# Kernel tuning notes

Hardware: AMD Instinct MI355X
Metric: run time of the kernel (lower is better)

Reference implementation:

```python
import jax, jax.numpy as jnp
import numpy as np

NUM_NODES = 512
HEADS = 4
IN_F = 256
OUT_F = 128
EPS = 1e-5


def _layernorm(x, g, b):
    mu = jnp.mean(x, axis=-1, keepdims=True)
    var = jnp.mean(jnp.square(x - mu), axis=-1, keepdims=True)
    return (x - mu) * jax.lax.rsqrt(var + EPS) * g + b


def setup_inputs() -> dict:
    key = jax.random.key(0)
    ks = jax.random.split(key, 16)
    N = 32 * NUM_NODES
    E = 262144
    s = 0.05
    return {
        "x": jax.random.normal(ks[0], (N, IN_F), jnp.float32),
        "edge_index": jax.random.randint(ks[1], (2, E), 0, N, jnp.int64),
        "W_l": jax.random.normal(ks[2], (IN_F, HEADS * OUT_F), jnp.float32) * s,
        "W_r": jax.random.normal(ks[3], (IN_F, HEADS * OUT_F), jnp.float32) * s,
        "att": jax.random.normal(ks[4], (HEADS, OUT_F), jnp.float32) * s,
        "gat_bias": jnp.zeros((OUT_F,), jnp.float32),
        "gat_gamma": jnp.ones((OUT_F,), jnp.float32),
        "gat_beta": jnp.zeros((OUT_F,), jnp.float32),
        "cnn_W": jax.random.normal(ks[5], (IN_F, OUT_F), jnp.float32) * s,
        "cnn_b": jnp.zeros((OUT_F,), jnp.float32),
        "conv_W": jax.random.normal(ks[6], (OUT_F, OUT_F, 7), jnp.float32) * s,
        "conv_b": jnp.zeros((OUT_F,), jnp.float32),
        "cnn_gamma": jnp.ones((OUT_F,), jnp.float32),
        "cnn_beta": jnp.zeros((OUT_F,), jnp.float32),
        "res_W": jax.random.normal(ks[7], (IN_F, OUT_F), jnp.float32) * s,
        "res_b": jnp.zeros((OUT_F,), jnp.float32),
        "fuse_gamma": jnp.ones((OUT_F,), jnp.float32),
        "fuse_beta": jnp.zeros((OUT_F,), jnp.float32),
    }


def reference(x, edge_index, W_l, W_r, att, gat_bias, gat_gamma, gat_beta,
              cnn_W, cnn_b, conv_W, conv_b, cnn_gamma, cnn_beta,
              res_W, res_b, fuse_gamma, fuse_beta):
    N = x.shape[0]
    B = N // NUM_NODES
    # --- GATv2 branch (add self-loops like PyG default) ---
    loop = jnp.arange(N, dtype=edge_index.dtype)
    src = jnp.concatenate([edge_index[0], loop])
    dst = jnp.concatenate([edge_index[1], loop])
    x_l = (x @ W_l).reshape(N, HEADS, OUT_F)
    x_r = (x @ W_r).reshape(N, HEADS, OUT_F)
    e = x_l[src] + x_r[dst]                      # [E+N, H, F]
    e = jnp.where(e > 0, e, 0.2 * e)             # leaky_relu, slope 0.2
    score = jnp.einsum('ehf,hf->eh', e, att)     # [E+N, H]
    m = jax.ops.segment_max(score, dst, num_segments=N)
    ex = jnp.exp(score - m[dst])
    denom = jax.ops.segment_sum(ex, dst, num_segments=N)
    alpha = ex / denom[dst]
    agg = jax.ops.segment_sum(alpha[:, :, None] * x_l[src], dst, num_segments=N)
    h_gat = jnp.mean(agg, axis=1) + gat_bias     # concat=False -> head mean
    h_gat = jnp.where(h_gat > 0, h_gat, 0.01 * h_gat)  # nn.LeakyReLU default
    h_gat = _layernorm(h_gat, gat_gamma, gat_beta)
    # --- CNN branch ---
    xc = x @ cnn_W + cnn_b                       # [N, F]
    xc = xc.reshape(B, NUM_NODES, OUT_F).transpose(0, 2, 1)  # [B, F, L]
    hc = jax.lax.conv_general_dilated(xc, conv_W, window_strides=(1,),
                                      padding=[(3, 3)],
                                      dimension_numbers=('NCW', 'OIW', 'NCW'))
    hc = hc + conv_b[None, :, None]
    hc = hc.transpose(0, 2, 1).reshape(N, OUT_F)
    hc = jax.nn.relu(hc)
    hc = _layernorm(hc, cnn_gamma, cnn_beta)
    # --- fuse + residual ---
    h = h_gat + hc + (x @ res_W + res_b)
    return _layernorm(h, fuse_gamma, fuse_beta)
```

## Files before the change

### kernel.cpp

```cpp
#include <hip/hip_runtime.h>
#include <hip/hip_bf16.h>
#include <math.h>

#define IN_F 256
#define OUT_F 128
#define HEADS 4
#define HF 512
#define NCAT 1280

typedef __hip_bfloat16 bf16;
typedef unsigned short ushort_t;

using bf16x8 = __attribute__((ext_vector_type(8))) short;
using f32x4  = __attribute__((ext_vector_type(4))) float;

__device__ __forceinline__ float bflo(unsigned u) { return __uint_as_float(u << 16); }
__device__ __forceinline__ float bfhi(unsigned u) { return __uint_as_float(u & 0xffff0000u); }
__device__ __forceinline__ float bf2f(ushort_t u) { return __uint_as_float((unsigned)u << 16); }
__device__ __forceinline__ ushort_t f2bf(float f) {
    __hip_bfloat16 h = __float2bfloat16(f);
    return *reinterpret_cast<ushort_t*>(&h);
}

__device__ __forceinline__ void gload16(const void* g, void* l) {
    __builtin_amdgcn_global_load_lds(
        (const __attribute__((address_space(1))) unsigned int*)g,
        (__attribute__((address_space(3))) unsigned int*)l, 16, 0, 0);
}

template <int CTRL>
__device__ __forceinline__ float dpp_add(float s) {
    int t = __builtin_amdgcn_update_dpp(0, __float_as_int(s), CTRL, 0xf, 0xf, true);
    return s + __int_as_float(t);
}
__device__ __forceinline__ float rowsum16(float s) {
    s = dpp_add<0x121>(s);
    s = dpp_add<0x122>(s);
    s = dpp_add<0x124>(s);
    s = dpp_add<0x128>(s);
    return s;
}

__global__ __launch_bounds__(256) void prep_kernel(
    const float* __restrict__ x, ushort_t* __restrict__ xb, int n_cvt,
    const float* __restrict__ Wl, const float* __restrict__ Wr,
    const float* __restrict__ Wc, const float* __restrict__ Wres,
    const float* __restrict__ Wconv,
    ushort_t* __restrict__ Wt, ushort_t* __restrict__ Wt2,
    const int* __restrict__ ei, int* __restrict__ counts, int E,
    int g1, int g2) {
    int b = blockIdx.x;
    if (b < g1) {
        int i = (b * 256 + threadIdx.x) * 8;
        if (i >= n_cvt) return;
        float4 a = *(const float4*)(x + i);
        float4 c = *(const float4*)(x + i + 4);
        uint4 o;
        o.x = f2bf(a.x) | ((unsigned)f2bf(a.y) << 16);
        o.y = f2bf(a.z) | ((unsigned)f2bf(a.w) << 16);
        o.z = f2bf(c.x) | ((unsigned)f2bf(c.y) << 16);
        o.w = f2bf(c.z) | ((unsigned)f2bf(c.w) << 16);
        *(uint4*)(xb + i) = o;
    } else if (b < g2) {
        int idx = (b - g1) * 256 + threadIdx.x;
        if (idx < NCAT * 256) {
            int n = idx >> 8, k = idx & 255;
            float v;
            if (n < 512)       v = Wl[(size_t)k * 512 + n];
            else if (n < 1024) v = Wr[(size_t)k * 512 + (n - 512)];
            else if (n < 1152) v = Wc[(size_t)k * 128 + (n - 1024)];
            else               v = Wres[(size_t)k * 128 + (n - 1152)];
            Wt[idx] = f2bf(v);
        } else {
            int j = idx - NCAT * 256;
            if (j < 7 * 128 * 128) {
                int k = j >> 14, o = (j >> 7) & 127, i = j & 127;
                Wt2[j] = f2bf(Wconv[((size_t)o * 128 + i) * 7 + k]);
            }
        }
    } else {
        int e = (b - g2) * 256 + threadIdx.x;
        if (e < E) atomicAdd(&counts[ei[E + e]], 1);
    }
}

__global__ __launch_bounds__(256) void mfma_gemm(
    const ushort_t* __restrict__ A,
    const ushort_t* __restrict__ Wt,
    ushort_t* __restrict__ xlb, ushort_t* __restrict__ xrb,
    ushort_t* __restrict__ xcb, ushort_t* __restrict__ resb,
    int M) {
    __shared__ __align__(1024) ushort_t As[128 * 64];
    __shared__ __align__(1024) ushort_t Bs[128 * 64];
    int tid = threadIdx.x;
    int lane = tid & 63, wid = tid >> 6;
    int wr = (wid >> 1) * 64, wc = (wid & 1) * 64;
    int brow = blockIdx.y * 128, bcol = blockIdx.x * 128;
    int srow = lane >> 3;
    int sslot = lane & 7;
    int rl = lane & 15, kq = lane >> 4;
    f32x4 acc[4][4] = {};
    for (int k0 = 0; k0 < 256; k0 += 64) {
        #pragma unroll
        for (int j = 0; j < 4; ++j) {
            int r = (wid * 4 + j) * 8 + srow;
            int sl = sslot ^ (r & 7);
            gload16(A  + (size_t)(brow + r) * 256 + k0 + sl * 8,
                    (char*)As + (wid * 4 + j) * 1024);
            gload16(Wt + (size_t)(bcol + r) * 256 + k0 + sl * 8,
                    (char*)Bs + (wid * 4 + j) * 1024);
        }
        __syncthreads();
        #pragma unroll
        for (int ks = 0; ks < 2; ++ks) {
            int cb = ks * 64 + kq * 16;
            bf16x8 af[4], bfv[4];
            #pragma unroll
            for (int m = 0; m < 4; ++m) {
                int r = wr + m * 16 + rl;
                af[m] = *(const bf16x8*)((const char*)As + r * 128 + (cb ^ ((r & 7) << 4)));
            }
            #pragma unroll
            for (int n = 0; n < 4; ++n) {
                int r = wc + n * 16 + rl;
                bfv[n] = *(const bf16x8*)((const char*)Bs + r * 128 + (cb ^ ((r & 7) << 4)));
            }
            #pragma unroll
            for (int m = 0; m < 4; ++m)
                #pragma unroll
                for (int n = 0; n < 4; ++n)
                    acc[m][n] = __builtin_amdgcn_mfma_f32_16x16x32_bf16(
                        af[m], bfv[n], acc[m][n], 0, 0, 0);
        }
        __syncthreads();
    }
    ushort_t* dstp; int cstride, cb2;
    if (bcol < 512)       { dstp = xlb;  cstride = 512; cb2 = bcol; }
    else if (bcol < 1024) { dstp = xrb;  cstride = 512; cb2 = bcol - 512; }
    else if (bcol < 1152) { dstp = xcb;  cstride = 128; cb2 = bcol - 1024; }
    else                  { dstp = resb; cstride = 128; cb2 = bcol - 1152; }
    int rowb = (lane >> 4) * 4;
    #pragma unroll
    for (int m = 0; m < 4; ++m)
        #pragma unroll
        for (int n = 0; n < 4; ++n) {
            int col = cb2 + wc + n * 16 + rl;
            #pragma unroll
            for (int q = 0; q < 4; ++q) {
                int row = brow + wr + m * 16 + rowb + q;
                dstp[(size_t)row * cstride + col] = f2bf(acc[m][n][q]);
            }
        }
}

__global__ __launch_bounds__(1024) void scan_kernel(
    const int* __restrict__ counts, int* __restrict__ offs,
    int* __restrict__ cursor, int N) {
    __shared__ int wsum[16];
    int t = threadIdx.x;
    int lane = t & 63, w = t >> 6;
    int base = t * 16;
    int local[16], s = 0;
    #pragma unroll
    for (int i = 0; i < 16; ++i) {
        int v = (base + i < N) ? counts[base + i] : 0;
        local[i] = v; s += v;
    }
    int sc = s;
    #pragma unroll
    for (int off = 1; off < 64; off <<= 1) {
        int v = __shfl_up(sc, off);
        if (lane >= off) sc += v;
    }
    if (lane == 63) wsum[w] = sc;
    __syncthreads();
    if (w == 0 && lane < 16) {
        int v = wsum[lane];
        int scv = v;
        #pragma unroll
        for (int off = 1; off < 16; off <<= 1) {
            int u = __shfl_up(scv, off);
            if (lane >= off) scv += u;
        }
        wsum[lane] = scv - v;
    }
    __syncthreads();
    int run = wsum[w] + sc - s;
    #pragma unroll
    for (int i = 0; i < 16; ++i) {
        if (base + i < N) { offs[base + i] = run; cursor[base + i] = run; }
        run += local[i];
    }
}

__global__ __launch_bounds__(256) void scatter_kernel(
    const int* __restrict__ ei, int* __restrict__ cursor,
    int* __restrict__ srcs, int E) {
    int e = blockIdx.x * 256 + threadIdx.x;
    if (e < E) {
        int d = ei[E + e];
        int p = atomicAdd(&cursor[d], 1);
        srcs[p] = ei[e];
    }
}

__global__ __launch_bounds__(256) void gat_fused_kernel(
    const ushort_t* __restrict__ xlb, const ushort_t* __restrict__ xrb,
    const int* __restrict__ srcs, const int* __restrict__ offs,
    const float* __restrict__ att, const float* __restrict__ gat_bias,
    const float* __restrict__ gat_gamma, const float* __restrict__ gat_beta,
    float* __restrict__ hgat_ln, int E, int N) {
    int wid = (blockIdx.x * 256 + threadIdx.x) >> 6;
    int lane = threadIdx.x & 63;
    if (wid >= N) return;
    int d = wid;
    const uint4 rv = ((const uint4*)(xrb + (size_t)d * HF))[lane];
    float xr8[8];
    xr8[0] = bflo(rv.x); xr8[1] = bfhi(rv.x);
    xr8[2] = bflo(rv.y); xr8[3] = bfhi(rv.y);
    xr8[4] = bflo(rv.z); xr8[5] = bfhi(rv.z);
    xr8[6] = bflo(rv.w); xr8[7] = bfhi(rv.w);
    const float LOG2E = 1.44269504f;
    const float4 a0 = ((const float4*)att)[lane * 2];
    const float4 a1 = ((const float4*)att)[lane * 2 + 1];
    const float aw[8] = {a0.x * LOG2E, a0.y * LOG2E, a0.z * LOG2E, a0.w * LOG2E,
                         a1.x * LOG2E, a1.y * LOG2E, a1.z * LOG2E, a1.w * LOG2E};
    float acc[8] = {};
    float dn = 0.f;

    auto process = [&](uint4 lv) {
        float xl8[8];
        xl8[0] = bflo(lv.x); xl8[1] = bfhi(lv.x);
        xl8[2] = bflo(lv.y); xl8[3] = bfhi(lv.y);
        xl8[4] = bflo(lv.z); xl8[5] = bfhi(lv.z);
        xl8[6] = bflo(lv.w); xl8[7] = bfhi(lv.w);
        float s1 = 0.f, s2 = 0.f;
        #pragma unroll
        for (int j = 0; j < 8; ++j) {
            float v = xl8[j] + xr8[j];
            s1 = fmaf(v, aw[j], s1);
            s2 = fmaf(fabsf(v), aw[j], s2);
        }
        float s = fmaf(0.6f, s1, 0.4f * s2);
        s = rowsum16(s);
        float ex = exp2f(s);
        dn += ex;
        #pragma unroll
        for (int j = 0; j < 8; ++j) acc[j] = fmaf(ex, xl8[j], acc[j]);
    };

    process(((const uint4*)(xlb + (size_t)d * HF))[lane]);

    int start = offs[d];
    int end = (d == N - 1) ? E : offs[d + 1];
    int p = start;
    for (; p + 3 < end; p += 4) {
        int s0 = srcs[p], s1 = srcs[p + 1], s2 = srcs[p + 2], s3 = srcs[p + 3];
        uint4 l0 = ((const uint4*)(xlb + (size_t)s0 * HF))[lane];
        uint4 l1 = ((const uint4*)(xlb + (size_t)s1 * HF))[lane];
        uint4 l2 = ((const uint4*)(xlb + (size_t)s2 * HF))[lane];
        uint4 l3 = ((const uint4*)(xlb + (size_t)s3 * HF))[lane];
        process(l0); process(l1); process(l2); process(l3);
    }
    for (; p < end; ++p)
        process(((const uint4*)(xlb + (size_t)srcs[p] * HF))[lane]);

    float inv = 1.f / dn;
    float v[8];
    #pragma unroll
    for (int j = 0; j < 8; ++j) {
        float t2 = acc[j] * inv;
        t2 += __shfl_xor(t2, 16);
        t2 += __shfl_xor(t2, 32);
        v[j] = t2;
    }
    int h = lane >> 4;
    int col = (lane & 15) * 8 + 2 * h;
    float g0 = 0.25f * v[2 * h]     + gat_bias[col];
    float g1 = 0.25f * v[2 * h + 1] + gat_bias[col + 1];
    g0 = g0 > 0.f ? g0 : 0.01f * g0;
    g1 = g1 > 0.f ? g1 : 0.01f * g1;
    float s = g0 + g1;
    #pragma unroll
    for (int off = 32; off; off >>= 1) s += __shfl_xor(s, off);
    float mu = s * (1.f / 128.f);
    float d0 = g0 - mu, d1 = g1 - mu;
    float vs = d0 * d0 + d1 * d1;
    #pragma unroll
    for (int off = 32; off; off >>= 1) vs += __shfl_xor(vs, off);
    float rinv = rsqrtf(vs * (1.f / 128.f) + 1e-5f);
    hgat_ln[(size_t)d * 128 + col]     = d0 * rinv * gat_gamma[col]     + gat_beta[col];
    hgat_ln[(size_t)d * 128 + col + 1] = d1 * rinv * gat_gamma[col + 1] + gat_beta[col + 1];
}

__global__ __launch_bounds__(256) void conv_fuse_kernel(
    const ushort_t* __restrict__ xcb, const float* __restrict__ cnn_b,
    const ushort_t* __restrict__ Wt2,
    const float* __restrict__ hgat_ln, const ushort_t* __restrict__ resb,
    const float* __restrict__ conv_b,
    const float* __restrict__ cnn_gamma, const float* __restrict__ cnn_beta,
    const float* __restrict__ res_b,
    const float* __restrict__ fuse_gamma, const float* __restrict__ fuse_beta,
    float* __restrict__ out) {
    __shared__ ushort_t As[38][136];
    __shared__ __align__(1024) ushort_t Bs[128 * 128];
    __shared__ float hbuf[32][129];
    int tid = threadIdx.x;
    int lane = tid & 63, wid = tid >> 6;
    int wr = (wid >> 1) * 16, wc = (wid & 1) * 64;
    int b = blockIdx.y, l0 = blockIdx.x * 32;
    for (int u = tid; u < 38 * 16; u += 256) {
        int r = u >> 4, seg = u & 15;
        int l = l0 - 3 + r;
        uint4 o4 = make_uint4(0, 0, 0, 0);
        if (l >= 0 && l < 512) {
            uint4 v = *(const uint4*)(xcb + (size_t)(b * 512 + l) * 128 + seg * 8);
            float4 b0 = *(const float4*)(cnn_b + seg * 8);
            float4 b1 = *(const float4*)(cnn_b + seg * 8 + 4);
            o4.x = f2bf(bflo(v.x) + b0.x) | ((unsigned)f2bf(bfhi(v.x) + b0.y) << 16);
            o4.y = f2bf(bflo(v.y) + b0.z) | ((unsigned)f2bf(bfhi(v.y) + b0.w) << 16);
            o4.z = f2bf(bflo(v.z) + b1.x) | ((unsigned)f2bf(bfhi(v.z) + b1.y) << 16);
            o4.w = f2bf(bflo(v.w) + b1.z) | ((unsigned)f2bf(bfhi(v.w) + b1.w) << 16);
        }
        *(uint4*)&As[r][seg * 8] = o4;
    }
    f32x4 acc[4] = {};
    int rl = lane & 15, kb = (lane >> 4) * 8;
    int sr4 = lane >> 4, ss = lane & 15;
    for (int k = 0; k < 7; ++k) {
        __syncthreads();
        #pragma unroll
        for (int j = 0; j < 8; ++j) {
            int r = (wid * 8 + j) * 4 + sr4;
            int sl = ss ^ (r & 15);
            gload16(Wt2 + ((size_t)(k * 128 + r)) * 128 + sl * 8,
                    (char*)Bs + (wid * 8 + j) * 1024);
        }
        __syncthreads();
        #pragma unroll
        for (int kk = 0; kk < 4; ++kk) {
            bf16x8 af = *(const bf16x8*)&As[wr + rl + k][kk * 32 + kb];
            int cbyte = kk * 64 + (lane >> 4) * 16;
            #pragma unroll
            for (int n = 0; n < 4; ++n) {
                int r = wc + n * 16 + rl;
                bf16x8 bfr = *(const bf16x8*)((const char*)Bs + r * 256
                                              + (cbyte ^ ((r & 15) << 4)));
                acc[n] = __builtin_amdgcn_mfma_f32_16x16x32_bf16(af, bfr, acc[n], 0, 0, 0);
            }
        }
    }
    __syncthreads();
    int rowb = (lane >> 4) * 4;
    #pragma unroll
    for (int n = 0; n < 4; ++n) {
        int col = wc + n * 16 + rl;
        float cb = conv_b[col];
        #pragma unroll
        for (int q = 0; q < 4; ++q) {
            int r = wr + rowb + q;
            hbuf[r][col] = fmaxf(acc[n][q] + cb, 0.f);
        }
    }
    __syncthreads();
    for (int r = wid * 8; r < wid * 8 + 8; ++r) {
        int grow = b * 512 + l0 + r;
        float h0 = hbuf[r][lane], h1 = hbuf[r][lane + 64];
        float s = h0 + h1;
        #pragma unroll
        for (int off = 32; off; off >>= 1) s += __shfl_xor(s, off);
        float mu = s * (1.f / 128.f);
        float d0 = h0 - mu, d1 = h1 - mu;
        float vs = d0 * d0 + d1 * d1;
        #pragma unroll
        for (int off = 32; off; off >>= 1) vs += __shfl_xor(vs, off);
        float inv = rsqrtf(vs * (1.f / 128.f) + 1e-5f);
        float hcn0 = d0 * inv * cnn_gamma[lane]      + cnn_beta[lane];
        float hcn1 = d1 * inv * cnn_gamma[lane + 64] + cnn_beta[lane + 64];
        size_t base = (size_t)grow * 128;
        float v0 = hgat_ln[base + lane]      + hcn0
                 + bf2f(resb[base + lane])      + res_b[lane];
        float v1 = hgat_ln[base + lane + 64] + hcn1
                 + bf2f(resb[base + lane + 64]) + res_b[lane + 64];
        s = v0 + v1;
        #pragma unroll
        for (int off = 32; off; off >>= 1) s += __shfl_xor(s, off);
        mu = s * (1.f / 128.f);
        d0 = v0 - mu; d1 = v1 - mu;
        vs = d0 * d0 + d1 * d1;
        #pragma unroll
        for (int off = 32; off; off >>= 1) vs += __shfl_xor(vs, off);
        inv = rsqrtf(vs * (1.f / 128.f) + 1e-5f);
        out[base + lane]      = d0 * inv * fuse_gamma[lane]      + fuse_beta[lane];
        out[base + lane + 64] = d1 * inv * fuse_gamma[lane + 64] + fuse_beta[lane + 64];
    }
}

extern "C" void kernel_launch(void* const* d_in, const int* in_sizes, int n_in,
                              void* d_out, int out_size, void* d_ws, size_t ws_size,
                              hipStream_t stream) {
    const float* x         = (const float*)d_in[0];
    const int*   ei        = (const int*)d_in[1];
    const float* W_l       = (const float*)d_in[2];
    const float* W_r       = (const float*)d_in[3];
    const float* att       = (const float*)d_in[4];
    const float* gat_bias  = (const float*)d_in[5];
    const float* gat_gamma = (const float*)d_in[6];
    const float* gat_beta  = (const float*)d_in[7];
    const float* cnn_W     = (const float*)d_in[8];
    const float* cnn_b     = (const float*)d_in[9];
    const float* conv_W    = (const float*)d_in[10];
    const float* conv_b    = (const float*)d_in[11];
    const float* cnn_gamma = (const float*)d_in[12];
    const float* cnn_beta  = (const float*)d_in[13];
    const float* res_W     = (const float*)d_in[14];
    const float* res_b     = (const float*)d_in[15];
    const float* fuse_gamma= (const float*)d_in[16];
    const float* fuse_beta = (const float*)d_in[17];

    int N = in_sizes[0] / IN_F;
    int E = in_sizes[1] / 2;

    char* ws = (char*)d_ws;
    size_t off = 0;
    ushort_t* xb     = (ushort_t*)(ws + off); off += (size_t)N * IN_F * 2;
    ushort_t* Wt     = (ushort_t*)(ws + off); off += (size_t)NCAT * IN_F * 2;
    ushort_t* Wt2    = (ushort_t*)(ws + off); off += (size_t)7 * 128 * 128 * 2;
    ushort_t* xlb    = (ushort_t*)(ws + off); off += (size_t)N * HF * 2;
    ushort_t* xrb    = (ushort_t*)(ws + off); off += (size_t)N * HF * 2;
    ushort_t* xcb    = (ushort_t*)(ws + off); off += (size_t)N * 128 * 2;
    ushort_t* resb   = (ushort_t*)(ws + off); off += (size_t)N * 128 * 2;
    int*  counts     = (int*)(ws + off);  off += (size_t)N * 4;
    int*  offs       = (int*)(ws + off);  off += (size_t)N * 4;
    int*  cursor     = (int*)(ws + off);  off += (size_t)N * 4;
    int*  srcs       = (int*)(ws + off);  off += (size_t)E * 4;
    float* hgat_ln   = (float*)(ws + off); off += (size_t)N * 128 * 4;

    hipMemsetAsync(counts, 0, (size_t)N * 4, stream);

    dim3 blk(256);
    int n_cvt = N * IN_F;
    int g1 = (n_cvt / 8 + 255) / 256;
    int g2 = g1 + (NCAT * 256 + 7 * 128 * 128 + 255) / 256;
    int g3 = g2 + (E + 255) / 256;
    prep_kernel<<<g3, blk, 0, stream>>>(x, xb, n_cvt,
        W_l, W_r, cnn_W, res_W, conv_W, Wt, Wt2, ei, counts, E, g1, g2);

    scan_kernel<<<1, 1024, 0, stream>>>(counts, offs, cursor, N);
    scatter_kernel<<<(E + 255) / 256, blk, 0, stream>>>(ei, cursor, srcs, E);

    mfma_gemm<<<dim3(NCAT / 128, N / 128), blk, 0, stream>>>(
        xb, Wt, xlb, xrb, xcb, resb, N);

    gat_fused_kernel<<<(N + 3) / 4, blk, 0, stream>>>(
        xlb, xrb, srcs, offs, att, gat_bias, gat_gamma, gat_beta, hgat_ln, E, N);

    conv_fuse_kernel<<<dim3(16, 32), blk, 0, stream>>>(
        xcb, cnn_b, Wt2, hgat_ln, resb, conv_b, cnn_gamma, cnn_beta,
        res_b, fuse_gamma, fuse_beta, (float*)d_out);
}
```

Measured before the change: 144.1 us.

## Reorder conv and GAT stages, fuse final layernorm into GAT kernel

Runs the conv+layernorm kernel first and writes its normalized output as bf16, then moves the residual add and final fuse layernorm into the GAT aggregation kernel. The fp32 hgat_ln intermediate is gone, so its write and re-read are no longer needed. The GAT inner math now uses two-wide float vectors, which may map to packed FMA instructions. The bf16 rounding of the CNN-branch output adds some precision loss.

Measured after the change: 142.9 us. No clear change (-0.8%).

```diff
diff --git a/kernel.cpp b/kernel.cpp
--- a/kernel.cpp
+++ b/kernel.cpp
@@ -13,6 +13,7 @@
 
 using bf16x8 = __attribute__((ext_vector_type(8))) short;
 using f32x4  = __attribute__((ext_vector_type(4))) float;
+using f32v2  = __attribute__((ext_vector_type(2))) float;
 
 __device__ __forceinline__ float bflo(unsigned u) { return __uint_as_float(u << 16); }
 __device__ __forceinline__ float bfhi(unsigned u) { return __uint_as_float(u & 0xffff0000u); }
@@ -204,104 +205,11 @@
     }
 }
 
-__global__ __launch_bounds__(256) void gat_fused_kernel(
-    const ushort_t* __restrict__ xlb, const ushort_t* __restrict__ xrb,
-    const int* __restrict__ srcs, const int* __restrict__ offs,
-    const float* __restrict__ att, const float* __restrict__ gat_bias,
-    const float* __restrict__ gat_gamma, const float* __restrict__ gat_beta,
-    float* __restrict__ hgat_ln, int E, int N) {
-    int wid = (blockIdx.x * 256 + threadIdx.x) >> 6;
-    int lane = threadIdx.x & 63;
-    if (wid >= N) return;
-    int d = wid;
-    const uint4 rv = ((const uint4*)(xrb + (size_t)d * HF))[lane];
-    float xr8[8];
-    xr8[0] = bflo(rv.x); xr8[1] = bfhi(rv.x);
-    xr8[2] = bflo(rv.y); xr8[3] = bfhi(rv.y);
-    xr8[4] = bflo(rv.z); xr8[5] = bfhi(rv.z);
-    xr8[6] = bflo(rv.w); xr8[7] = bfhi(rv.w);
-    const float LOG2E = 1.44269504f;
-    const float4 a0 = ((const float4*)att)[lane * 2];
-    const float4 a1 = ((const float4*)att)[lane * 2 + 1];
-    const float aw[8] = {a0.x * LOG2E, a0.y * LOG2E, a0.z * LOG2E, a0.w * LOG2E,
-                         a1.x * LOG2E, a1.y * LOG2E, a1.z * LOG2E, a1.w * LOG2E};
-    float acc[8] = {};
-    float dn = 0.f;
-
-    auto process = [&](uint4 lv) {
-        float xl8[8];
-        xl8[0] = bflo(lv.x); xl8[1] = bfhi(lv.x);
-        xl8[2] = bflo(lv.y); xl8[3] = bfhi(lv.y);
-        xl8[4] = bflo(lv.z); xl8[5] = bfhi(lv.z);
-        xl8[6] = bflo(lv.w); xl8[7] = bfhi(lv.w);
-        float s1 = 0.f, s2 = 0.f;
-        #pragma unroll
-        for (int j = 0; j < 8; ++j) {
-            float v = xl8[j] + xr8[j];
-            s1 = fmaf(v, aw[j], s1);
-            s2 = fmaf(fabsf(v), aw[j], s2);
-        }
-        float s = fmaf(0.6f, s1, 0.4f * s2);
-        s = rowsum16(s);
-        float ex = exp2f(s);
-        dn += ex;
-        #pragma unroll
-        for (int j = 0; j < 8; ++j) acc[j] = fmaf(ex, xl8[j], acc[j]);
-    };
-
-    process(((const uint4*)(xlb + (size_t)d * HF))[lane]);
-
-    int start = offs[d];
-    int end = (d == N - 1) ? E : offs[d + 1];
-    int p = start;
-    for (; p + 3 < end; p += 4) {
-        int s0 = srcs[p], s1 = srcs[p + 1], s2 = srcs[p + 2], s3 = srcs[p + 3];
-        uint4 l0 = ((const uint4*)(xlb + (size_t)s0 * HF))[lane];
-        uint4 l1 = ((const uint4*)(xlb + (size_t)s1 * HF))[lane];
-        uint4 l2 = ((const uint4*)(xlb + (size_t)s2 * HF))[lane];
-        uint4 l3 = ((const uint4*)(xlb + (size_t)s3 * HF))[lane];
-        process(l0); process(l1); process(l2); process(l3);
-    }
-    for (; p < end; ++p)
-        process(((const uint4*)(xlb + (size_t)srcs[p] * HF))[lane]);
-
-    float inv = 1.f / dn;
-    float v[8];
-    #pragma unroll
-    for (int j = 0; j < 8; ++j) {
-        float t2 = acc[j] * inv;
-        t2 += __shfl_xor(t2, 16);
-        t2 += __shfl_xor(t2, 32);
-        v[j] = t2;
-    }
-    int h = lane >> 4;
-    int col = (lane & 15) * 8 + 2 * h;
-    float g0 = 0.25f * v[2 * h]     + gat_bias[col];
-    float g1 = 0.25f * v[2 * h + 1] + gat_bias[col + 1];
-    g0 = g0 > 0.f ? g0 : 0.01f * g0;
-    g1 = g1 > 0.f ? g1 : 0.01f * g1;
-    float s = g0 + g1;
-    #pragma unroll
-    for (int off = 32; off; off >>= 1) s += __shfl_xor(s, off);
-    float mu = s * (1.f / 128.f);
-    float d0 = g0 - mu, d1 = g1 - mu;
-    float vs = d0 * d0 + d1 * d1;
-    #pragma unroll
-    for (int off = 32; off; off >>= 1) vs += __shfl_xor(vs, off);
-    float rinv = rsqrtf(vs * (1.f / 128.f) + 1e-5f);
-    hgat_ln[(size_t)d * 128 + col]     = d0 * rinv * gat_gamma[col]     + gat_beta[col];
-    hgat_ln[(size_t)d * 128 + col + 1] = d1 * rinv * gat_gamma[col + 1] + gat_beta[col + 1];
-}
-
-__global__ __launch_bounds__(256) void conv_fuse_kernel(
+__global__ __launch_bounds__(256) void conv_ln_kernel(
     const ushort_t* __restrict__ xcb, const float* __restrict__ cnn_b,
-    const ushort_t* __restrict__ Wt2,
-    const float* __restrict__ hgat_ln, const ushort_t* __restrict__ resb,
-    const float* __restrict__ conv_b,
+    const ushort_t* __restrict__ Wt2, const float* __restrict__ conv_b,
     const float* __restrict__ cnn_gamma, const float* __restrict__ cnn_beta,
-    const float* __restrict__ res_b,
-    const float* __restrict__ fuse_gamma, const float* __restrict__ fuse_beta,
-    float* __restrict__ out) {
+    ushort_t* __restrict__ hcn_ln) {
     __shared__ ushort_t As[38][136];
     __shared__ __align__(1024) ushort_t Bs[128 * 128];
     __shared__ float hbuf[32][129];
@@ -375,25 +283,121 @@
         #pragma unroll
         for (int off = 32; off; off >>= 1) vs += __shfl_xor(vs, off);
         float inv = rsqrtf(vs * (1.f / 128.f) + 1e-5f);
-        float hcn0 = d0 * inv * cnn_gamma[lane]      + cnn_beta[lane];
-        float hcn1 = d1 * inv * cnn_gamma[lane + 64] + cnn_beta[lane + 64];
         size_t base = (size_t)grow * 128;
-        float v0 = hgat_ln[base + lane]      + hcn0
-                 + bf2f(resb[base + lane])      + res_b[lane];
-        float v1 = hgat_ln[base + lane + 64] + hcn1
-                 + bf2f(resb[base + lane + 64]) + res_b[lane + 64];
-        s = v0 + v1;
-        #pragma unroll
-        for (int off = 32; off; off >>= 1) s += __shfl_xor(s, off);
-        mu = s * (1.f / 128.f);
-        d0 = v0 - mu; d1 = v1 - mu;
-        vs = d0 * d0 + d1 * d1;
-        #pragma unroll
-        for (int off = 32; off; off >>= 1) vs += __shfl_xor(vs, off);
-        inv = rsqrtf(vs * (1.f / 128.f) + 1e-5f);
-        out[base + lane]      = d0 * inv * fuse_gamma[lane]      + fuse_beta[lane];
-        out[base + lane + 64] = d1 * inv * fuse_gamma[lane + 64] + fuse_beta[lane + 64];
-    }
+        hcn_ln[base + lane]      = f2bf(d0 * inv * cnn_gamma[lane]      + cnn_beta[lane]);
+        hcn_ln[base + lane + 64] = f2bf(d1 * inv * cnn_gamma[lane + 64] + cnn_beta[lane + 64]);
+    }
+}
+
+__global__ __launch_bounds__(256) void gat_final_kernel(
+    const ushort_t* __restrict__ xlb, const ushort_t* __restrict__ xrb,
+    const int* __restrict__ srcs, const int* __restrict__ offs,
+    const float* __restrict__ att, const float* __restrict__ gat_bias,
+    const float* __restrict__ gat_gamma, const float* __restrict__ gat_beta,
+    const ushort_t* __restrict__ hcn_ln, const ushort_t* __restrict__ resb,
+    const float* __restrict__ res_b,
+    const float* __restrict__ fuse_gamma, const float* __restrict__ fuse_beta,
+    float* __restrict__ out, int E, int N) {
+    int wid = (blockIdx.x * 256 + threadIdx.x) >> 6;
+    int lane = threadIdx.x & 63;
+    if (wid >= N) return;
+    int d = wid;
+    const uint4 rv = ((const uint4*)(xrb + (size_t)d * HF))[lane];
+    f32v2 xr2[4];
+    xr2[0] = f32v2{bflo(rv.x), bfhi(rv.x)};
+    xr2[1] = f32v2{bflo(rv.y), bfhi(rv.y)};
+    xr2[2] = f32v2{bflo(rv.z), bfhi(rv.z)};
+    xr2[3] = f32v2{bflo(rv.w), bfhi(rv.w)};
+    const float LOG2E = 1.44269504f;
+    const float4 a0 = ((const float4*)att)[lane * 2];
+    const float4 a1 = ((const float4*)att)[lane * 2 + 1];
+    f32v2 aw2[4] = {f32v2{a0.x, a0.y} * LOG2E, f32v2{a0.z, a0.w} * LOG2E,
+                    f32v2{a1.x, a1.y} * LOG2E, f32v2{a1.z, a1.w} * LOG2E};
+    f32v2 acc2[4] = {};
+    float dn = 0.f;
+
+    auto process = [&](uint4 lv) {
+        f32v2 xl2[4];
+        xl2[0] = f32v2{bflo(lv.x), bfhi(lv.x)};
+        xl2[1] = f32v2{bflo(lv.y), bfhi(lv.y)};
+        xl2[2] = f32v2{bflo(lv.z), bfhi(lv.z)};
+        xl2[3] = f32v2{bflo(lv.w), bfhi(lv.w)};
+        f32v2 s1 = {0.f, 0.f}, s2 = {0.f, 0.f};
+        #pragma unroll
+        for (int j = 0; j < 4; ++j) {
+            f32v2 v = xl2[j] + xr2[j];
+            s1 = __builtin_elementwise_fma(v, aw2[j], s1);
+            s2 = __builtin_elementwise_fma(__builtin_elementwise_abs(v), aw2[j], s2);
+        }
+        float s = fmaf(0.6f, s1.x + s1.y, 0.4f * (s2.x + s2.y));
+        s = rowsum16(s);
+        float ex = exp2f(s);
+        dn += ex;
+        f32v2 exv = {ex, ex};
+        #pragma unroll
+        for (int j = 0; j < 4; ++j)
+            acc2[j] = __builtin_elementwise_fma(exv, xl2[j], acc2[j]);
+    };
+
+    process(((const uint4*)(xlb + (size_t)d * HF))[lane]);
+
+    int start = offs[d];
+    int end = (d == N - 1) ? E : offs[d + 1];
+    int p = start;
+    for (; p + 3 < end; p += 4) {
+        int s0 = srcs[p], s1 = srcs[p + 1], s2 = srcs[p + 2], s3 = srcs[p + 3];
+        uint4 l0 = ((const uint4*)(xlb + (size_t)s0 * HF))[lane];
+        uint4 l1 = ((const uint4*)(xlb + (size_t)s1 * HF))[lane];
+        uint4 l2 = ((const uint4*)(xlb + (size_t)s2 * HF))[lane];
+        uint4 l3 = ((const uint4*)(xlb + (size_t)s3 * HF))[lane];
+        process(l0); process(l1); process(l2); process(l3);
+    }
+    for (; p < end; ++p)
+        process(((const uint4*)(xlb + (size_t)srcs[p] * HF))[lane]);
+
+    float inv = 1.f / dn;
+    float v[8];
+    #pragma unroll
+    for (int j = 0; j < 4; ++j) {
+        float tx = acc2[j].x * inv, ty = acc2[j].y * inv;
+        tx += __shfl_xor(tx, 16); tx += __shfl_xor(tx, 32);
+        ty += __shfl_xor(ty, 16); ty += __shfl_xor(ty, 32);
+        v[2 * j] = tx; v[2 * j + 1] = ty;
+    }
+    int h = lane >> 4;
+    int col = (lane & 15) * 8 + 2 * h;
+    float g0 = 0.25f * v[2 * h]     + gat_bias[col];
+    float g1 = 0.25f * v[2 * h + 1] + gat_bias[col + 1];
+    g0 = g0 > 0.f ? g0 : 0.01f * g0;
+    g1 = g1 > 0.f ? g1 : 0.01f * g1;
+    float s = g0 + g1;
+    #pragma unroll
+    for (int off = 32; off; off >>= 1) s += __shfl_xor(s, off);
+    float mu = s * (1.f / 128.f);
+    float d0 = g0 - mu, d1 = g1 - mu;
+    float vs = d0 * d0 + d1 * d1;
+    #pragma unroll
+    for (int off = 32; off; off >>= 1) vs += __shfl_xor(vs, off);
+    float rinv = rsqrtf(vs * (1.f / 128.f) + 1e-5f);
+    float hg0 = d0 * rinv * gat_gamma[col]     + gat_beta[col];
+    float hg1 = d1 * rinv * gat_gamma[col + 1] + gat_beta[col + 1];
+    size_t base = (size_t)d * 128 + col;
+    unsigned hcu = *(const unsigned*)(hcn_ln + base);
+    unsigned rsu = *(const unsigned*)(resb + base);
+    float v0 = hg0 + bflo(hcu) + bflo(rsu) + res_b[col];
+    float v1 = hg1 + bfhi(hcu) + bfhi(rsu) + res_b[col + 1];
+    s = v0 + v1;
+    #pragma unroll
+    for (int off = 32; off; off >>= 1) s += __shfl_xor(s, off);
+    mu = s * (1.f / 128.f);
+    d0 = v0 - mu; d1 = v1 - mu;
+    vs = d0 * d0 + d1 * d1;
+    #pragma unroll
+    for (int off = 32; off; off >>= 1) vs += __shfl_xor(vs, off);
+    rinv = rsqrtf(vs * (1.f / 128.f) + 1e-5f);
+    float2 o2 = make_float2(d0 * rinv * fuse_gamma[col]     + fuse_beta[col],
+                            d1 * rinv * fuse_gamma[col + 1] + fuse_beta[col + 1]);
+    *(float2*)(out + base) = o2;
 }
 
 extern "C" void kernel_launch(void* const* d_in, const int* in_sizes, int n_in,
@@ -430,11 +434,11 @@
     ushort_t* xrb    = (ushort_t*)(ws + off); off += (size_t)N * HF * 2;
     ushort_t* xcb    = (ushort_t*)(ws + off); off += (size_t)N * 128 * 2;
     ushort_t* resb   = (ushort_t*)(ws + off); off += (size_t)N * 128 * 2;
+    ushort_t* hcn_ln = (ushort_t*)(ws + off); off += (size_t)N * 128 * 2;
     int*  counts     = (int*)(ws + off);  off += (size_t)N * 4;
     int*  offs       = (int*)(ws + off);  off += (size_t)N * 4;
     int*  cursor     = (int*)(ws + off);  off += (size_t)N * 4;
     int*  srcs       = (int*)(ws + off);  off += (size_t)E * 4;
-    float* hgat_ln   = (float*)(ws + off); off += (size_t)N * 128 * 4;
 
     hipMemsetAsync(counts, 0, (size_t)N * 4, stream);
 
@@ -452,10 +456,10 @@
     mfma_gemm<<<dim3(NCAT / 128, N / 128), blk, 0, stream>>>(
         xb, Wt, xlb, xrb, xcb, resb, N);
 
-    gat_fused_kernel<<<(N + 3) / 4, blk, 0, stream>>>(
-        xlb, xrb, srcs, offs, att, gat_bias, gat_gamma, gat_beta, hgat_ln, E, N);
-
-    conv_fuse_kernel<<<dim3(16, 32), blk, 0, stream>>>(
-        xcb, cnn_b, Wt2, hgat_ln, resb, conv_b, cnn_gamma, cnn_beta,
-        res_b, fuse_gamma, fuse_beta, (float*)d_out);
-}
+    conv_ln_kernel<<<dim3(16, 32), blk, 0, stream>>>(
+        xcb, cnn_b, Wt2, conv_b, cnn_gamma, cnn_beta, hcn_ln);
+
+    gat_final_kernel<<<(N + 3) / 4, blk, 0, stream>>>(
+        xlb, xrb, srcs, offs, att, gat_bias, gat_gamma, gat_beta,
+        hcn_ln, resb, res_b, fuse_gamma, fuse_beta, (float*)d_out, E, N);
+}
```
